# Kernel optimization log

Hardware: AMD Instinct MI355X
Metric: run time of the kernel (lower is better)

## Reference

```python
import jax, jax.numpy as jnp
import numpy as np

EPS = 1e-5      # BatchNorm eps (eval mode, running stats at init: mean=0, var=1)
SLOPE = 0.2     # LeakyReLU negative slope


def _knn_idx(x, k):
    # x: (B, N, D) -> (B, N, k) indices of k nearest neighbors (squared L2, feature space)
    sq = jnp.sum(x * x, axis=-1)                              # (B, N)
    dist = sq[:, :, None] + sq[:, None, :] - 2.0 * jnp.einsum('bnd,bmd->bnm', x, x)
    return jax.lax.top_k(-dist, k)[1]                         # nearest = largest of -dist


def _bn_lrelu(y, gamma, beta):
    # eval BatchNorm with running_mean=0, running_var=1, then LeakyReLU(0.2)
    y = y * (gamma / jnp.sqrt(1.0 + EPS)) + beta
    return jnp.where(y >= 0, y, SLOPE * y)


def _edge_conv(x, W, gamma, beta, k):
    # x: (B, N, D); W: (C_out, 2D). Returns (B, N, C_out) after max over k neighbors.
    idx = _knn_idx(x, k)                                      # (B, N, k)
    nb = jax.vmap(lambda xt, i: xt[i])(x, idx)                # (B, N, k, D) neighbor gather
    ctr = jnp.broadcast_to(x[:, :, None, :], nb.shape)
    feat = jnp.concatenate([nb - ctr, ctr], axis=-1)          # (B, N, k, 2D)
    y = jnp.einsum('bnkd,od->bnko', feat, W)                  # 1x1 conv (no bias)
    y = _bn_lrelu(y, gamma, beta)
    return jnp.max(y, axis=2)                                 # max-pool over neighbors


def setup_inputs() -> dict:
    key = jax.random.key(0)
    ks = jax.random.split(key, 16)
    B, N, k, out_dim = 8, 4096, 20, 512
    x = jax.random.normal(ks[0], (B, 3, N), dtype=jnp.float32)
    dims = [(64, 6), (64, 128), (128, 128), (256, 256), (out_dim, 512)]
    inp = {'x': x, 'k': k}
    for i, (co, ci) in enumerate(dims, start=1):
        inp[f'W{i}'] = jax.random.normal(ks[3 * i - 2], (co, ci), dtype=jnp.float32) * (1.0 / np.sqrt(ci))
        inp[f'g{i}'] = jax.random.uniform(ks[3 * i - 1], (co,), dtype=jnp.float32, minval=0.5, maxval=1.5)
        inp[f'b{i}'] = 0.1 * jax.random.normal(ks[3 * i], (co,), dtype=jnp.float32)
    return inp


def reference(x, W1, g1, b1, W2, g2, b2, W3, g3, b3, W4, g4, b4, W5, g5, b5, k):
    xt = jnp.transpose(x, (0, 2, 1))                          # (B, N, 3)
    x1 = _edge_conv(xt, W1, g1, b1, k)                        # (B, N, 64)
    x2 = _edge_conv(x1, W2, g2, b2, k)                        # (B, N, 64)
    x3 = _edge_conv(x2, W3, g3, b3, k)                        # (B, N, 128)
    x4 = _edge_conv(x3, W4, g4, b4, k)                        # (B, N, 256)
    h = jnp.concatenate([x1, x2, x3, x4], axis=-1)            # (B, N, 512)
    y = _bn_lrelu(jnp.einsum('bnd,od->bno', h, W5), g5, b5)   # (B, N, out_dim)
    return jnp.concatenate([jnp.max(y, axis=1), jnp.mean(y, axis=1)], axis=-1)  # (B, 2*out_dim)
```

## Files before the change

kernel.cpp:

```cpp
#include <hip/hip_runtime.h>
#include <math.h>

#define BATCH 8
#define N_PTS 4096
#define KNN 20
#define EPS_BN 1e-5f
#define SLOPE 0.2f
#define M_ROWS (BATCH * N_PTS)

typedef __attribute__((ext_vector_type(8))) short short8;
typedef __attribute__((ext_vector_type(4))) float float4v;
typedef __attribute__((ext_vector_type(16))) float float16v;

__device__ __forceinline__ unsigned short f2bf(float f) {
    unsigned u = __float_as_uint(f);
    unsigned r = (u + 0x7FFFu + ((u >> 16) & 1u)) >> 16;
    return (unsigned short)r;
}
__device__ __forceinline__ float bf2f(unsigned short h) {
    return __uint_as_float((unsigned)h << 16);
}

__global__ void convert_x1(const float* __restrict__ x,
                           unsigned short* __restrict__ xh, unsigned short* __restrict__ xl,
                           float* __restrict__ sq) {
    int i = blockIdx.x * blockDim.x + threadIdx.x;
    if (i >= M_ROWS) return;
    int b = i / N_PTS, n = i % N_PTS;
    float v[3], s = 0.f;
    #pragma unroll
    for (int d = 0; d < 3; ++d) {
        v[d] = x[((size_t)b * 3 + d) * N_PTS + n];
        s += v[d] * v[d];
    }
    sq[i] = s;
    #pragma unroll
    for (int d = 0; d < 32; ++d) {
        float f = (d < 3) ? v[d] : 0.f;
        unsigned short h = f2bf(f);
        xh[(size_t)i * 32 + d] = h;
        xl[(size_t)i * 32 + d] = f2bf(f - bf2f(h));
    }
}

__global__ void sqnorm_hl(const unsigned short* __restrict__ hh,
                          const unsigned short* __restrict__ hl,
                          int D, float* __restrict__ sq) {
    int w = threadIdx.x >> 6, lane = threadIdx.x & 63;
    int row = blockIdx.x * 4 + w;
    if (row >= M_ROWS) return;
    const unsigned short* ph = hh + (size_t)row * 512;
    const unsigned short* pl = hl + (size_t)row * 512;
    float s = 0.f;
    for (int d = lane; d < D; d += 64) {
        float v = bf2f(ph[d]) + bf2f(pl[d]);
        s += v * v;
    }
    #pragma unroll
    for (int off = 32; off > 0; off >>= 1) s += __shfl_down(s, off, 64);
    if (lane == 0) sq[row] = s;
}

__global__ void repack_edge_split(const float* __restrict__ W, int Co, int D, int KP,
                                  unsigned short* __restrict__ Wh, unsigned short* __restrict__ Wl) {
    int i = blockIdx.x * blockDim.x + threadIdx.x;
    int tot = 2 * Co * KP;
    if (i >= tot) return;
    int r = i / KP, d = i % KP;
    float v = 0.f;
    if (d < D) v = (r < Co) ? W[(size_t)r * 2 * D + d] : W[(size_t)(r - Co) * 2 * D + D + d];
    unsigned short h = f2bf(v);
    Wh[i] = h; Wl[i] = f2bf(v - bf2f(h));
}

__global__ void repack_w5_split(const float* __restrict__ W,
                                unsigned short* __restrict__ Wh, unsigned short* __restrict__ Wl) {
    int i = blockIdx.x * blockDim.x + threadIdx.x;
    if (i >= 512 * 512) return;
    float v = W[i];
    unsigned short h = f2bf(v);
    Wh[i] = h; Wl[i] = f2bf(v - bf2f(h));
}

template<int DPAD>
__launch_bounds__(256, 2)
__global__ void knn_mfma(const unsigned short* __restrict__ Xh,
                         const unsigned short* __restrict__ Xl,
                         int strideX,
                         const float* __restrict__ sq, int* __restrict__ idxout) {
    constexpr int KS16 = DPAD / 16;
    constexpr int SST  = 33;
    constexpr size_t POOL = (size_t)64 * 4 * KNN * 4 * 2;
    __shared__ __align__(16) char smem[POOL];
    float* Sfw = (float*)smem + (size_t)(threadIdx.x >> 6) * 32 * SST;
    float*    kb = (float*)smem;
    unsigned* ib = (unsigned*)(kb + 64 * 4 * KNN);

    const int b = blockIdx.y;
    const int row0 = blockIdx.x * 64;
    const int tid = threadIdx.x;
    const int w = tid >> 6, lane = tid & 63;
    const int l31 = lane & 31, lh = lane >> 5;
    const int rbase = (w & 1) * 32;
    const int cb32  = (w >> 1) * 32;

    const unsigned short* Xhb = Xh + (size_t)b * N_PTS * strideX;
    const unsigned short* Xlb = Xl + (size_t)b * N_PTS * strideX;
    const float* sqb = sq + (size_t)b * N_PTS;

    short8 ah[KS16], al[KS16];
    #pragma unroll
    for (int ks = 0; ks < KS16; ++ks) {
        size_t o = (size_t)(row0 + rbase + l31) * strideX + ks * 16 + lh * 8;
        ah[ks] = *(const short8*)(Xhb + o);
        al[ks] = *(const short8*)(Xlb + o);
    }

    const unsigned short* pBh = Xhb + (size_t)(cb32 + l31) * strideX + lh * 8;
    const unsigned short* pBl = Xlb + (size_t)(cb32 + l31) * strideX + lh * 8;
    const float* psq = sqb + cb32 + l31;

    float fv[KNN]; int fi[KNN];
    #pragma unroll
    for (int p = 0; p < KNN; ++p) { fv[p] = INFINITY; fi[p] = 0x7FFFFFFF; }

    for (int c0 = 0; c0 < N_PTS; c0 += 64) {
        short8 bh[KS16], bl[KS16];
        #pragma unroll
        for (int ks = 0; ks < KS16; ++ks) {
            bh[ks] = *(const short8*)(pBh + (size_t)c0 * strideX + ks * 16);
            bl[ks] = *(const short8*)(pBl + (size_t)c0 * strideX + ks * 16);
        }
        float sc = psq[c0];

        float16v a0 = {}, a1 = {}, a2 = {};
        #pragma unroll
        for (int ks = 0; ks < KS16; ++ks) {
            if (KS16 <= 4) {
                a0 = __builtin_amdgcn_mfma_f32_32x32x16_bf16(ah[ks], bh[ks], a0, 0, 0, 0);
                a1 = __builtin_amdgcn_mfma_f32_32x32x16_bf16(al[ks], bh[ks], a1, 0, 0, 0);
                a2 = __builtin_amdgcn_mfma_f32_32x32x16_bf16(ah[ks], bl[ks], a2, 0, 0, 0);
            } else {
                a0 = __builtin_amdgcn_mfma_f32_32x32x16_bf16(ah[ks], bh[ks], a0, 0, 0, 0);
                a0 = __builtin_amdgcn_mfma_f32_32x32x16_bf16(al[ks], bh[ks], a0, 0, 0, 0);
                a0 = __builtin_amdgcn_mfma_f32_32x32x16_bf16(ah[ks], bl[ks], a0, 0, 0, 0);
            }
        }

        #pragma unroll
        for (int reg = 0; reg < 16; ++reg) {
            int rowL = (reg & 3) + 8 * (reg >> 2) + 4 * lh;
            float v = (KS16 <= 4) ? (a0[reg] + a1[reg] + a2[reg]) : a0[reg];
            Sfw[rowL * SST + l31] = sc - 2.f * v;
        }
        asm volatile("s_waitcnt lgkmcnt(0)" ::: "memory");

        float f19 = fv[KNN - 1];
        float fT = fminf(f19, __shfl_xor(f19, 32, 64));

        const int sbase = l31 * SST + lh * 16;
        unsigned mask = 0;
        #pragma unroll
        for (int jj = 0; jj < 16; ++jj) {
            float v = Sfw[sbase + jj];
            if (v < f19 && v <= fT) mask |= (1u << jj);
        }
        while (mask) {
            int jj = __ffs(mask) - 1;
            mask &= mask - 1;
            float v = Sfw[sbase + jj];
            if (v < fv[KNN - 1]) {
                fv[KNN - 1] = v;
                fi[KNN - 1] = c0 + cb32 + lh * 16 + jj;
                #pragma unroll
                for (int p = KNN - 1; p > 0; --p) {
                    float va = fv[p - 1], vb = fv[p];
                    int   ia = fi[p - 1], ic = fi[p];
                    bool sw = vb < va;
                    fv[p - 1] = sw ? vb : va; fv[p] = sw ? va : vb;
                    fi[p - 1] = sw ? ic : ia; fi[p] = sw ? ia : ic;
                }
            }
        }
    }

    __syncthreads();
    {
        int rowb = rbase + l31;
        int slot = (w >> 1) * 2 + lh;
        int base = (rowb * 4 + slot) * KNN;
        #pragma unroll
        for (int p = 0; p < KNN; ++p) { kb[base + p] = fv[p]; ib[base + p] = (unsigned)fi[p]; }
    }
    __syncthreads();
    if (tid < 64) {
        int base = tid * 4 * KNN;
        #pragma unroll
        for (int p = 0; p < KNN; ++p) { fv[p] = kb[base + p]; fi[p] = (int)ib[base + p]; }
        #pragma unroll 1
        for (int qq = 0; qq < 3 * KNN; ++qq) {
            float    v  = kb[base + KNN + qq];
            unsigned ii = ib[base + KNN + qq];
            bool ins = (v < fv[KNN - 1]) ||
                       (v == fv[KNN - 1] && (int)ii < fi[KNN - 1]);
            if (ins) {
                fv[KNN - 1] = v; fi[KNN - 1] = (int)ii;
                #pragma unroll
                for (int p = KNN - 1; p > 0; --p) {
                    float va = fv[p - 1], vb = fv[p];
                    int   ia = fi[p - 1], ic = fi[p];
                    bool sw = (vb < va) || (vb == va && ic < ia);
                    fv[p - 1] = sw ? vb : va; fv[p] = sw ? va : vb;
                    fi[p - 1] = sw ? ic : ia; fi[p] = sw ? ia : ic;
                }
            }
        }
        int* op = idxout + ((size_t)(b * N_PTS + row0 + tid)) * KNN;
        #pragma unroll
        for (int p = 0; p < KNN; ++p) op[p] = fi[p];
    }
}

__launch_bounds__(256)
__global__ void fgemm(const unsigned short* __restrict__ Ah, const unsigned short* __restrict__ Al,
                      int strideA, int K,
                      const unsigned short* __restrict__ Wh, const unsigned short* __restrict__ Wl,
                      int C, float* __restrict__ out, int fuse_bn,
                      const float* __restrict__ g, const float* __restrict__ beta) {
    __shared__ unsigned short AhS[128 * 40];
    __shared__ unsigned short AlS[128 * 40];
    __shared__ unsigned short BhS[128 * 40];
    __shared__ unsigned short BlS[128 * 40];

    const int c0 = blockIdx.x * 128;
    const int m0 = blockIdx.y * 128;
    const int tid = threadIdx.x;
    const int w = tid >> 6, lane = tid & 63;
    const int n = lane & 15, q = lane >> 4;

    float4v acc[2][8];
    #pragma unroll
    for (int rt = 0; rt < 2; ++rt)
        #pragma unroll
        for (int ct = 0; ct < 8; ++ct) acc[rt][ct] = (float4v){0.f, 0.f, 0.f, 0.f};

    for (int kk = 0; kk < K; kk += 32) {
        __syncthreads();
        for (int tt = tid; tt < 512; tt += 256) {
            int rr = tt >> 2, c8 = tt & 3;
            size_t oa = (size_t)(m0 + rr) * strideA + kk + c8 * 8;
            *(short8*)&AhS[rr * 40 + c8 * 8] = *(const short8*)(Ah + oa);
            *(short8*)&AlS[rr * 40 + c8 * 8] = *(const short8*)(Al + oa);
            size_t ob = (size_t)(c0 + rr) * K + kk + c8 * 8;
            *(short8*)&BhS[rr * 40 + c8 * 8] = *(const short8*)(Wh + ob);
            *(short8*)&BlS[rr * 40 + c8 * 8] = *(const short8*)(Wl + ob);
        }
        __syncthreads();

        short8 af[2][2];
        #pragma unroll
        for (int rt = 0; rt < 2; ++rt) {
            af[rt][0] = *(const short8*)&AhS[(w * 32 + rt * 16 + n) * 40 + q * 8];
            af[rt][1] = *(const short8*)&AlS[(w * 32 + rt * 16 + n) * 40 + q * 8];
        }
        #pragma unroll
        for (int ct = 0; ct < 8; ++ct) {
            short8 bh = *(const short8*)&BhS[(ct * 16 + n) * 40 + q * 8];
            short8 bl = *(const short8*)&BlS[(ct * 16 + n) * 40 + q * 8];
            #pragma unroll
            for (int rt = 0; rt < 2; ++rt) {
                acc[rt][ct] = __builtin_amdgcn_mfma_f32_16x16x32_bf16(af[rt][0], bh, acc[rt][ct], 0, 0, 0);
                acc[rt][ct] = __builtin_amdgcn_mfma_f32_16x16x32_bf16(af[rt][1], bh, acc[rt][ct], 0, 0, 0);
                acc[rt][ct] = __builtin_amdgcn_mfma_f32_16x16x32_bf16(af[rt][0], bl, acc[rt][ct], 0, 0, 0);
            }
        }
    }

    #pragma unroll
    for (int rt = 0; rt < 2; ++rt)
        #pragma unroll
        for (int ct = 0; ct < 8; ++ct) {
            int c = c0 + ct * 16 + n;
            float sc = 1.f, bt = 0.f;
            if (fuse_bn) { sc = g[c] / sqrtf(1.f + EPS_BN); bt = beta[c]; }
            #pragma unroll
            for (int e = 0; e < 4; ++e) {
                int m = m0 + w * 32 + rt * 16 + q * 4 + e;
                float v = acc[rt][ct][e];
                if (fuse_bn) { v = v * sc + bt; v = (v >= 0.f) ? v : SLOPE * v; }
                out[(size_t)m * C + c] = v;
            }
        }
}

__global__ void pool_kernel(const float* __restrict__ zc2, int Co,
                            const int* __restrict__ idx,
                            const float* __restrict__ g, const float* __restrict__ beta,
                            unsigned short* __restrict__ hh, unsigned short* __restrict__ hl,
                            int hoff) {
    int n = blockIdx.x, b = blockIdx.y;
    int o = threadIdx.x;
    size_t bn = (size_t)b * N_PTS + n;
    const int* ip = idx + bn * KNN;
    float zn   = zc2[bn * (size_t)(2 * Co) + o];
    float base = zc2[bn * (size_t)(2 * Co) + Co + o] - zn;
    float m = -INFINITY;
    #pragma unroll
    for (int j = 0; j < KNN; ++j) {
        size_t rr = (size_t)b * N_PTS + ip[j];
        m = fmaxf(m, zc2[rr * (size_t)(2 * Co) + o]);
    }
    float y = m + base;
    float sc = g[o] / sqrtf(1.f + EPS_BN);
    y = y * sc + beta[o];
    y = (y >= 0.f) ? y : SLOPE * y;
    unsigned short h = f2bf(y);
    hh[bn * 512 + hoff + o] = h;
    hl[bn * 512 + hoff + o] = f2bf(y - bf2f(h));
}

__global__ void reduce_partial(const float* __restrict__ y5,
                               float* __restrict__ pmax, float* __restrict__ psum) {
    int chunk = blockIdx.x, b = blockIdx.y, c = threadIdx.x;
    float mx = -INFINITY, sm = 0.f;
    for (int qq = 0; qq < 128; ++qq) {
        int n = chunk * 128 + qq;
        float v = y5[((size_t)b * N_PTS + n) * 512 + c];
        mx = fmaxf(mx, v);
        sm += v;
    }
    pmax[((size_t)b * 32 + chunk) * 512 + c] = mx;
    psum[((size_t)b * 32 + chunk) * 512 + c] = sm;
}

__global__ void reduce_final(const float* __restrict__ pmax,
                             const float* __restrict__ psum,
                             float* __restrict__ out) {
    int i = blockIdx.x * blockDim.x + threadIdx.x;
    if (i >= BATCH * 512) return;
    int b = i / 512, c = i % 512;
    float mx = -INFINITY, sm = 0.f;
    for (int qq = 0; qq < 32; ++qq) {
        mx = fmaxf(mx, pmax[((size_t)b * 32 + qq) * 512 + c]);
        sm += psum[((size_t)b * 32 + qq) * 512 + c];
    }
    out[(size_t)b * 1024 + c] = mx;
    out[(size_t)b * 1024 + 512 + c] = sm * (1.f / 4096.f);
}

extern "C" void kernel_launch(void* const* d_in, const int* in_sizes, int n_in,
                              void* d_out, int out_size, void* d_ws, size_t ws_size,
                              hipStream_t stream) {
    const float* x = (const float*)d_in[0];
    const float* W[5], *gg[5], *bb[5];
    for (int i = 0; i < 5; ++i) {
        W[i]  = (const float*)d_in[2 + 3 * i];
        gg[i] = (const float*)d_in[3 + 3 * i];
        bb[i] = (const float*)d_in[4 + 3 * i];
    }
    float* outp = (float*)d_out;

    char* wsb = (char*)d_ws;
    size_t off = 0;
    unsigned short* x1h = (unsigned short*)(wsb + off); off += (size_t)M_ROWS * 32 * 2;
    unsigned short* x1l = (unsigned short*)(wsb + off); off += (size_t)M_ROWS * 32 * 2;
    float* sq = (float*)(wsb + off); off += (size_t)M_ROWS * 4;
    int*   idx = (int*)(wsb + off); off += (size_t)M_ROWS * KNN * 4;
    unsigned short* Wh = (unsigned short*)(wsb + off); off += (size_t)512 * 512 * 2;
    unsigned short* Wl = (unsigned short*)(wsb + off); off += (size_t)512 * 512 * 2;
    unsigned short* hh = (unsigned short*)(wsb + off); off += (size_t)M_ROWS * 512 * 2;
    unsigned short* hl = (unsigned short*)(wsb + off); off += (size_t)M_ROWS * 512 * 2;
    float* zc2 = (float*)(wsb + off); off += (size_t)M_ROWS * 512 * 4;
    float* pmx = (float*)(wsb + off); off += (size_t)BATCH * 32 * 512 * 4;
    float* psm = (float*)(wsb + off); off += (size_t)BATCH * 32 * 512 * 4;
    (void)ws_size; (void)in_sizes; (void)n_in; (void)out_size;

    convert_x1<<<(M_ROWS + 255) / 256, 256, 0, stream>>>(x, x1h, x1l, sq);

    struct L { int D, Co, KP, hoff; };
    const L layers[4] = { {3, 64, 32, 0}, {64, 64, 64, 64}, {64, 128, 64, 128}, {128, 256, 128, 256} };

    for (int li = 0; li < 4; ++li) {
        const L& ly = layers[li];
        const unsigned short* Ahp;
        const unsigned short* Alp;
        int strideA;
        if (li == 0) { Ahp = x1h; Alp = x1l; strideA = 32; }
        else {
            int po = layers[li - 1].hoff;
            Ahp = hh + po; Alp = hl + po; strideA = 512;
            sqnorm_hl<<<M_ROWS / 4, 256, 0, stream>>>(Ahp, Alp, ly.D, sq);
        }

        if (li == 0)
            knn_mfma<32><<<dim3(N_PTS / 64, BATCH), 256, 0, stream>>>(Ahp, Alp, strideA, sq, idx);
        else if (ly.D == 64)
            knn_mfma<64><<<dim3(N_PTS / 64, BATCH), 256, 0, stream>>>(Ahp, Alp, strideA, sq, idx);
        else
            knn_mfma<128><<<dim3(N_PTS / 64, BATCH), 256, 0, stream>>>(Ahp, Alp, strideA, sq, idx);

        repack_edge_split<<<(2 * ly.Co * ly.KP + 255) / 256, 256, 0, stream>>>(
            W[li], ly.Co, ly.D, ly.KP, Wh, Wl);
        fgemm<<<dim3((2 * ly.Co) / 128, M_ROWS / 128), 256, 0, stream>>>(
            Ahp, Alp, strideA, ly.KP, Wh, Wl, 2 * ly.Co, zc2, 0, nullptr, nullptr);
        pool_kernel<<<dim3(N_PTS, BATCH), ly.Co, 0, stream>>>(
            zc2, ly.Co, idx, gg[li], bb[li], hh, hl, ly.hoff);
    }

    repack_w5_split<<<(512 * 512 + 255) / 256, 256, 0, stream>>>(W[4], Wh, Wl);
    fgemm<<<dim3(4, M_ROWS / 128), 256, 0, stream>>>(
        hh, hl, 512, 512, Wh, Wl, 512, zc2, 1, gg[4], bb[4]);

    reduce_partial<<<dim3(32, BATCH), 512, 0, stream>>>(zc2, pmx, psm);
    reduce_final<<<(BATCH * 512 + 255) / 256, 256, 0, stream>>>(pmx, psm, outp);
}
```

Measured before the change: 1.474 ms.

## Prefetch next KNN tile, share 4-way thresholds via LDS, vectorize candidate reads

The KNN kernel is restructured into a two-stage loop that prefetches the next 64-column B tile into registers while the current tile is processed (for small feature dims). The pruning threshold is now shared across all four column slots through an LDS array instead of a single lane shuffle. Candidate scores are read once as float2 vectors and selected from registers with a select tree instead of re-reading LDS. The extra registers and unsynchronized LDS threshold reads may lower occupancy or give stale, looser thresholds.

```diff
diff --git a/kernel.cpp b/kernel.cpp
--- a/kernel.cpp
+++ b/kernel.cpp
@@ -9,6 +9,7 @@
 #define M_ROWS (BATCH * N_PTS)
 
 typedef __attribute__((ext_vector_type(8))) short short8;
+typedef __attribute__((ext_vector_type(2))) float float2v;
 typedef __attribute__((ext_vector_type(4))) float float4v;
 typedef __attribute__((ext_vector_type(16))) float float16v;
 
@@ -89,10 +90,14 @@
                          int strideX,
                          const float* __restrict__ sq, int* __restrict__ idxout) {
     constexpr int KS16 = DPAD / 16;
-    constexpr int SST  = 33;
-    constexpr size_t POOL = (size_t)64 * 4 * KNN * 4 * 2;
+    constexpr bool PF  = (KS16 <= 4);
+    constexpr int SST  = 34;
+    constexpr size_t SFB   = (size_t)4 * 32 * SST * 4;
+    constexpr size_t MERGE = (size_t)64 * 4 * KNN * 4 * 2;
+    constexpr size_t POOL  = (SFB + 256 * 4) > MERGE ? (SFB + 256 * 4) : MERGE;
     __shared__ __align__(16) char smem[POOL];
-    float* Sfw = (float*)smem + (size_t)(threadIdx.x >> 6) * 32 * SST;
+    float* Sfw  = (float*)smem + (size_t)(threadIdx.x >> 6) * 32 * SST;
+    float* thrT = (float*)smem + (size_t)4 * 32 * SST;
     float*    kb = (float*)smem;
     unsigned* ib = (unsigned*)(kb + 64 * 4 * KNN);
 
@@ -103,6 +108,8 @@
     const int l31 = lane & 31, lh = lane >> 5;
     const int rbase = (w & 1) * 32;
     const int cb32  = (w >> 1) * 32;
+    const int rowb  = rbase + l31;
+    const int slot  = (w >> 1) * 2 + lh;
 
     const unsigned short* Xhb = Xh + (size_t)b * N_PTS * strideX;
     const unsigned short* Xlb = Xl + (size_t)b * N_PTS * strideX;
@@ -124,54 +131,96 @@
     #pragma unroll
     for (int p = 0; p < KNN; ++p) { fv[p] = INFINITY; fi[p] = 0x7FFFFFFF; }
 
-    for (int c0 = 0; c0 < N_PTS; c0 += 64) {
-        short8 bh[KS16], bl[KS16];
+    thrT[tid] = INFINITY;
+    __syncthreads();
+
+    short8 bhA[KS16], blA[KS16], bhB[KS16], blB[KS16];
+    if constexpr (PF) {
         #pragma unroll
         for (int ks = 0; ks < KS16; ++ks) {
-            bh[ks] = *(const short8*)(pBh + (size_t)c0 * strideX + ks * 16);
-            bl[ks] = *(const short8*)(pBl + (size_t)c0 * strideX + ks * 16);
+            bhA[ks] = *(const short8*)(pBh + ks * 16);
+            blA[ks] = *(const short8*)(pBl + ks * 16);
+        }
+    }
+
+    auto body = [&](short8 (&bch)[KS16], short8 (&bcl)[KS16],
+                    short8 (&bnh)[KS16], short8 (&bnl)[KS16], int c0) {
+        if constexpr (!PF) {
+            #pragma unroll
+            for (int ks = 0; ks < KS16; ++ks) {
+                bch[ks] = *(const short8*)(pBh + (size_t)c0 * strideX + ks * 16);
+                bcl[ks] = *(const short8*)(pBl + (size_t)c0 * strideX + ks * 16);
+            }
+        } else {
+            int cp = (c0 + 64 < N_PTS) ? c0 + 64 : 0;
+            #pragma unroll
+            for (int ks = 0; ks < KS16; ++ks) {
+                bnh[ks] = *(const short8*)(pBh + (size_t)cp * strideX + ks * 16);
+                bnl[ks] = *(const short8*)(pBl + (size_t)cp * strideX + ks * 16);
+            }
         }
         float sc = psq[c0];
 
         float16v a0 = {}, a1 = {}, a2 = {};
         #pragma unroll
         for (int ks = 0; ks < KS16; ++ks) {
-            if (KS16 <= 4) {
-                a0 = __builtin_amdgcn_mfma_f32_32x32x16_bf16(ah[ks], bh[ks], a0, 0, 0, 0);
-                a1 = __builtin_amdgcn_mfma_f32_32x32x16_bf16(al[ks], bh[ks], a1, 0, 0, 0);
-                a2 = __builtin_amdgcn_mfma_f32_32x32x16_bf16(ah[ks], bl[ks], a2, 0, 0, 0);
+            if constexpr (PF) {
+                a0 = __builtin_amdgcn_mfma_f32_32x32x16_bf16(ah[ks], bch[ks], a0, 0, 0, 0);
+                a1 = __builtin_amdgcn_mfma_f32_32x32x16_bf16(al[ks], bch[ks], a1, 0, 0, 0);
+                a2 = __builtin_amdgcn_mfma_f32_32x32x16_bf16(ah[ks], bcl[ks], a2, 0, 0, 0);
             } else {
-                a0 = __builtin_amdgcn_mfma_f32_32x32x16_bf16(ah[ks], bh[ks], a0, 0, 0, 0);
-                a0 = __builtin_amdgcn_mfma_f32_32x32x16_bf16(al[ks], bh[ks], a0, 0, 0, 0);
-                a0 = __builtin_amdgcn_mfma_f32_32x32x16_bf16(ah[ks], bl[ks], a0, 0, 0, 0);
+                a0 = __builtin_amdgcn_mfma_f32_32x32x16_bf16(ah[ks], bch[ks], a0, 0, 0, 0);
+                a1 = __builtin_amdgcn_mfma_f32_32x32x16_bf16(al[ks], bch[ks], a1, 0, 0, 0);
+                a0 = __builtin_amdgcn_mfma_f32_32x32x16_bf16(ah[ks], bcl[ks], a0, 0, 0, 0);
             }
         }
 
         #pragma unroll
         for (int reg = 0; reg < 16; ++reg) {
             int rowL = (reg & 3) + 8 * (reg >> 2) + 4 * lh;
-            float v = (KS16 <= 4) ? (a0[reg] + a1[reg] + a2[reg]) : a0[reg];
-            Sfw[rowL * SST + l31] = sc - 2.f * v;
+            float acv = PF ? (a0[reg] + a1[reg] + a2[reg]) : (a0[reg] + a1[reg]);
+            Sfw[rowL * SST + l31] = sc - 2.f * acv;
         }
         asm volatile("s_waitcnt lgkmcnt(0)" ::: "memory");
 
+        float fT = fminf(fminf(thrT[rowb], thrT[64 + rowb]),
+                         fminf(thrT[128 + rowb], thrT[192 + rowb]));
         float f19 = fv[KNN - 1];
-        float fT = fminf(f19, __shfl_xor(f19, 32, 64));
 
         const int sbase = l31 * SST + lh * 16;
+        float2v c2[8];
+        #pragma unroll
+        for (int u = 0; u < 8; ++u) c2[u] = *(const float2v*)&Sfw[sbase + 2 * u];
         unsigned mask = 0;
         #pragma unroll
-        for (int jj = 0; jj < 16; ++jj) {
-            float v = Sfw[sbase + jj];
-            if (v < f19 && v <= fT) mask |= (1u << jj);
-        }
+        for (int u = 0; u < 8; ++u) {
+            if (c2[u][0] < f19 && c2[u][0] <= fT) mask |= (1u << (2 * u));
+            if (c2[u][1] < f19 && c2[u][1] <= fT) mask |= (1u << (2 * u + 1));
+        }
+
+        const int cidx = c0 + cb32 + lh * 16;
         while (mask) {
             int jj = __ffs(mask) - 1;
             mask &= mask - 1;
-            float v = Sfw[sbase + jj];
+            bool j1 = jj & 1, j2 = jj & 2, j4 = jj & 4, j8 = jj & 8;
+            float t0 = j1 ? c2[0][1] : c2[0][0];
+            float t1 = j1 ? c2[1][1] : c2[1][0];
+            float t2 = j1 ? c2[2][1] : c2[2][0];
+            float t3 = j1 ? c2[3][1] : c2[3][0];
+            float t4 = j1 ? c2[4][1] : c2[4][0];
+            float t5 = j1 ? c2[5][1] : c2[5][0];
+            float t6 = j1 ? c2[6][1] : c2[6][0];
+            float t7 = j1 ? c2[7][1] : c2[7][0];
+            float u0 = j2 ? t1 : t0;
+            float u1 = j2 ? t3 : t2;
+            float u2 = j2 ? t5 : t4;
+            float u3 = j2 ? t7 : t6;
+            float r0 = j4 ? u1 : u0;
+            float r1 = j4 ? u3 : u2;
+            float v  = j8 ? r1 : r0;
             if (v < fv[KNN - 1]) {
                 fv[KNN - 1] = v;
-                fi[KNN - 1] = c0 + cb32 + lh * 16 + jj;
+                fi[KNN - 1] = cidx + jj;
                 #pragma unroll
                 for (int p = KNN - 1; p > 0; --p) {
                     float va = fv[p - 1], vb = fv[p];
@@ -182,12 +231,18 @@
                 }
             }
         }
+
+        thrT[slot * 64 + rowb] = fv[KNN - 1];
+    };
+
+    #pragma unroll 1
+    for (int c0 = 0; c0 < N_PTS; c0 += 128) {
+        body(bhA, blA, bhB, blB, c0);
+        body(bhB, blB, bhA, blA, c0 + 64);
     }
 
     __syncthreads();
     {
-        int rowb = rbase + l31;
-        int slot = (w >> 1) * 2 + lh;
         int base = (rowb * 4 + slot) * KNN;
         #pragma unroll
         for (int p = 0; p < KNN; ++p) { kb[base + p] = fv[p]; ib[base + p] = (unsigned)fi[p]; }
```

Measured after the change: 1.500 ms. No clear change (+1.8%).
